# Kernel tuning notes

Measured on AMD Instinct MI355X. Metric: run time of the kernel, lower is better.

## Reference

```python
import jax, jax.numpy as jnp
import numpy as np

N, E, S, K, NB = 16384, 262144, 10, 64, 8
R_MAX, P_CUT, AVG_NEIGH = 5.0, 5, 16.0
L_OF_LM = np.array([0, 1, 1, 1, 2, 2, 2, 2, 2])  # l value of each of the 9 lm components
L_SLICES = [(0, 1), (1, 4), (4, 9)]               # lm ranges for l = 0,1,2
MLP_H = 16


def _sph(u):
    # real spherical harmonics up to l=2, e3nn 'component' normalization (sum_m Y_lm^2 = 2l+1)
    x, y, z = u[..., 0], u[..., 1], u[..., 2]
    s3, s15, s5 = np.float32(np.sqrt(3.0)), np.float32(np.sqrt(15.0)), np.float32(np.sqrt(5.0))
    return jnp.stack([
        jnp.ones_like(x),
        s3 * x, s3 * y, s3 * z,
        s15 * x * y, s15 * y * z, (s5 / 2) * (3 * z * z - 1), s15 * x * z, (s15 / 2) * (x * x - y * y),
    ], axis=-1)


def _radial(r):
    # Bessel radial basis with smooth polynomial cutoff envelope (p = P_CUT)
    u = r / R_MAX
    r_safe = jnp.where(r > 1e-9, r, 1.0)
    n = jnp.arange(1, NB + 1, dtype=r.dtype)
    bess = np.float32(np.sqrt(2.0 / R_MAX)) * jnp.sin(n * jnp.pi * u[:, None]) / r_safe[:, None]
    p = float(P_CUT)
    env = 1.0 - (p + 1) * (p + 2) / 2 * u**P_CUT + p * (p + 2) * u**(P_CUT + 1) - p * (p + 1) / 2 * u**(P_CUT + 2)
    env = jnp.where(u < 1.0, env, 0.0)
    return bess * env[:, None]  # [E, NB]


def setup_inputs() -> dict:
    key = jax.random.key(0)
    ks = jax.random.split(key, 16)
    positions = jax.random.uniform(ks[0], (N, 3), jnp.float32) * 4.0  # box so many edges fall inside r_max
    species = jax.random.randint(ks[1], (N,), 0, S)
    senders = jax.random.randint(ks[2], (E,), 0, N)
    receivers = jax.random.randint(ks[3], (E,), 0, N)
    shifts = jnp.zeros((E, 3), jnp.float32)
    W_embed = jax.random.normal(ks[4], (S, K), jnp.float32)
    W_rad = jax.random.normal(ks[5], (2, 3, NB, K), jnp.float32) * 0.3
    W_mix = jax.random.normal(ks[6], (2, 3, K, K), jnp.float32) / np.sqrt(K)
    W_prod = jax.random.normal(ks[7], (2, 3, 3, K), jnp.float32) * 0.1
    W_sc = jax.random.normal(ks[8], (2, S, 3, K, K), jnp.float32) / np.sqrt(K)
    W_ro0 = jax.random.normal(ks[9], (K,), jnp.float32) / np.sqrt(K)
    W_m1 = jax.random.normal(ks[10], (K, MLP_H), jnp.float32) / np.sqrt(K)
    b_m1 = jnp.zeros((MLP_H,), jnp.float32)
    W_m2 = jax.random.normal(ks[11], (MLP_H,), jnp.float32) / np.sqrt(MLP_H)
    return dict(positions=positions, shifts=shifts, species=species, senders=senders,
                receivers=receivers, W_embed=W_embed, W_rad=W_rad, W_mix=W_mix,
                W_prod=W_prod, W_sc=W_sc, W_ro0=W_ro0, W_m1=W_m1, b_m1=b_m1, W_m2=W_m2)


def reference(positions, shifts, species, senders, receivers, W_embed, W_rad, W_mix,
              W_prod, W_sc, W_ro0, W_m1, b_m1, W_m2):
    lm = jnp.asarray(L_OF_LM)
    onehot = jax.nn.one_hot(species, S, dtype=positions.dtype)
    # node embedding: scalars only -> feats [N, 9(lm), K]
    feats = jnp.zeros((N, 9, K), positions.dtype).at[:, 0, :].set(onehot @ W_embed)

    # edge geometry
    vec = positions[receivers] - positions[senders] + shifts           # [E, 3]
    r = jnp.linalg.norm(vec, axis=-1)                                  # [E]
    u_hat = vec / jnp.where(r > 1e-9, r, 1.0)[:, None]
    Y = _sph(u_hat)                                                     # [E, 9]
    rad = _radial(r)                                                    # [E, NB]

    energies = []
    for i in range(2):
        # interaction: radial-weighted SH messages from sender scalars, scatter-sum to receivers
        hs = feats[:, 0, :][senders]                                    # [E, K]
        Rl = jnp.einsum('eb,lbk->elk', rad, W_rad[i])[:, lm, :]         # [E, 9, K]
        msg = hs[:, None, :] * Y[:, :, None] * Rl                       # [E, 9, K]
        A = jax.ops.segment_sum(msg, receivers, num_segments=N) / AVG_NEIGH
        A = jnp.einsum('nmk,mkj->nmj', A, W_mix[i][lm])                 # per-l channel mixing

        # correlation-3 equivariant product basis (symmetric-contraction style)
        A0 = A[:, 0, :]
        inv = jnp.sum(A * A, axis=1)                                    # rotation-invariant [N, K]
        w1, w2, w3 = (W_prod[i, j][lm] for j in range(3))               # each [9, K]
        B = A * (w1[None] + w2[None] * A0[:, None, :] + w3[None] * inv[:, None, :])

        # species-dependent self-connection (linear of feats x node_attrs), per-l weights
        sc = jnp.concatenate([
            jnp.einsum('nmk,ns,skj->nmj', feats[:, st:en], onehot, W_sc[i, :, l])
            for l, (st, en) in enumerate(L_SLICES)], axis=1)
        feats = B + sc

        if i == 0:
            energies.append(feats[:, 0, :] @ W_ro0)                     # linear readout
        else:
            feats = feats.at[:, 1:, :].set(0.0)                         # last layer keeps 0e only
            energies.append(jax.nn.silu(feats[:, 0, :] @ W_m1 + b_m1) @ W_m2)

    return jnp.stack(energies, axis=1)  # [N, num_interactions]
```

## Files before the change

kernel.cpp:

```cpp
#include <hip/hip_runtime.h>

#define NN 16384
#define NE 262144
#define NSPEC 10
#define KC 64
#define MLPH 16
#define SEG 128
#define EPSG 2048
#define SC_BPS 160

typedef float v2f __attribute__((ext_vector_type(2)));

__device__ __forceinline__ float wave_reduce(float v) {
#pragma unroll
    for (int off = 32; off > 0; off >>= 1) v += __shfl_down(v, off, 64);
    return v;
}

__device__ __forceinline__ float f4c(const float4& v, int j) {
    const float* p = &v.x;
    return p[j];
}

__global__ void __launch_bounds__(1024) k_pre(
    const float* __restrict__ W_embed,
    const int* __restrict__ species,
    const int* __restrict__ receivers,
    int* __restrict__ eslot,
    unsigned short* __restrict__ cnt16,
    float4* __restrict__ h04) {
    __shared__ int cntL[NN];
    int t = threadIdx.x;
#pragma unroll
    for (int i = 0; i < 16; ++i) cntL[t + 1024 * i] = 0;
    __syncthreads();
    int ebase = blockIdx.x * EPSG;
#pragma unroll
    for (int j = 0; j < EPSG / 1024; ++j) {
        int e = ebase + j * 1024 + t;
        int r = receivers[e];
        eslot[e] = atomicAdd(&cntL[r], 1);
    }
    int gt = blockIdx.x * 1024 + t;
#pragma unroll
    for (int q = 0; q < 2; ++q) {
        int idx = gt * 2 + q;
        int n = idx >> 4, w = idx & 15;
        h04[idx] = reinterpret_cast<const float4*>(W_embed + species[n] * KC)[w];
    }
    __syncthreads();
    unsigned short* o = cnt16 + (size_t)blockIdx.x * NN;
#pragma unroll
    for (int i = 0; i < 16; ++i)
        o[t + 1024 * i] = (unsigned short)cntL[t + 1024 * i];
}

__global__ void __launch_bounds__(128) k_colscan(
    const unsigned short* __restrict__ cnt16,
    int* __restrict__ seg_base,
    int* __restrict__ count) {
    int r = blockIdx.x * 128 + threadIdx.x;
    int run = 0;
#pragma unroll 4
    for (int g = 0; g < SEG; ++g) {
        int c = cnt16[(size_t)g * NN + r];
        seg_base[(size_t)g * NN + r] = run;
        run += c;
    }
    count[r] = run;
}

__global__ void __launch_bounds__(1024) k_scan(
    const int* __restrict__ count, int* __restrict__ row_start,
    const int* __restrict__ species, int* __restrict__ nslot,
    int* __restrict__ sp_start) {
    __shared__ int lds[1024];
    __shared__ int itercnt[256 * NSPEC];
    __shared__ int spt[NSPEC];
    int t = threadIdx.x;
    int lane = t & 63;
    int w = t >> 6;
#pragma unroll
    for (int j = 0; j < 16; ++j) {
        int n = w * 1024 + j * 64 + lane;
        int sp = species[n];
#pragma unroll
        for (int s = 0; s < NSPEC; ++s) {
            unsigned long long mask = __ballot(sp == s);
            if (lane == 0) itercnt[(w * 16 + j) * NSPEC + s] = (int)__popcll(mask);
        }
    }
    int base = t * 16;
    int local[16];
    int ssum = 0;
#pragma unroll
    for (int b = 0; b < 16; ++b) { local[b] = count[base + b]; ssum += local[b]; }
    lds[t] = ssum;
    __syncthreads();
    for (int off = 1; off < 1024; off <<= 1) {
        int v = (t >= off) ? lds[t - off] : 0;
        __syncthreads();
        lds[t] += v;
        __syncthreads();
    }
    int run = lds[t] - ssum;
#pragma unroll
    for (int b = 0; b < 16; ++b) { row_start[base + b] = run; run += local[b]; }
    if (t == 1023) row_start[NN] = run;
    __syncthreads();
    if (w < NSPEC) {
        int s = w;
        int v0 = itercnt[(lane * 4 + 0) * NSPEC + s];
        int v1 = itercnt[(lane * 4 + 1) * NSPEC + s];
        int v2 = itercnt[(lane * 4 + 2) * NSPEC + s];
        int v3 = itercnt[(lane * 4 + 3) * NSPEC + s];
        int ls = v0 + v1 + v2 + v3;
        int inc = ls;
#pragma unroll
        for (int off = 1; off < 64; off <<= 1) {
            int v = __shfl_up(inc, off, 64);
            if (lane >= off) inc += v;
        }
        int exc = inc - ls;
        itercnt[(lane * 4 + 0) * NSPEC + s] = exc;
        itercnt[(lane * 4 + 1) * NSPEC + s] = exc + v0;
        itercnt[(lane * 4 + 2) * NSPEC + s] = exc + v0 + v1;
        itercnt[(lane * 4 + 3) * NSPEC + s] = exc + v0 + v1 + v2;
        if (lane == 63) spt[s] = inc;
    }
    __syncthreads();
    if (t == 0) {
        int r2 = 0;
        for (int s = 0; s < NSPEC; ++s) { sp_start[s] = r2; r2 += spt[s]; }
        sp_start[NSPEC] = r2;
    }
    __syncthreads();
#pragma unroll
    for (int j = 0; j < 16; ++j) {
        int n = w * 1024 + j * 64 + lane;
        int sp = species[n];
        int rank = 0;
#pragma unroll
        for (int s = 0; s < NSPEC; ++s) {
            unsigned long long mask = __ballot(sp == s);
            if (sp == s)
                rank = (int)__popcll(mask & ((1ull << lane) - 1ull));
        }
        nslot[n] = itercnt[(w * 16 + j) * NSPEC + sp] + rank;
    }
}

__global__ void k_geom(const float* __restrict__ pos,
                       const float* __restrict__ shifts,
                       const int* __restrict__ senders,
                       const int* __restrict__ receivers,
                       const int* __restrict__ row_start,
                       const int* __restrict__ seg_base,
                       const int* __restrict__ eslot,
                       const int* __restrict__ species,
                       const int* __restrict__ sp_start,
                       const int* __restrict__ nslot,
                       int* __restrict__ ord,
                       float* __restrict__ edgerec,
                       int* __restrict__ ssend) {
    int e = blockIdx.x * 256 + threadIdx.x;
    if (e < NN) {
        int sp = species[e];
        ord[sp_start[sp] + nslot[e]] = e;
    }
    int s = senders[e], r = receivers[e];
    float dx = pos[r * 3 + 0] - pos[s * 3 + 0] + shifts[e * 3 + 0];
    float dy = pos[r * 3 + 1] - pos[s * 3 + 1] + shifts[e * 3 + 1];
    float dz = pos[r * 3 + 2] - pos[s * 3 + 2] + shifts[e * 3 + 2];
    float rn = sqrtf(dx * dx + dy * dy + dz * dz);
    float den = (rn > 1e-9f) ? rn : 1.0f;
    float x = dx / den, y = dy / den, z = dz / den;
    const float s3  = 1.7320508075688772f;
    const float s15 = 3.8729833462074170f;
    const float s5h = 1.1180339887498949f;
    const float s15h = 1.9364916731037085f;
    float rec[16];
    rec[0] = s3 * x;
    rec[1] = s3 * y;
    rec[2] = s3 * z;
    rec[3] = s15 * x * y;
    rec[4] = s15 * y * z;
    rec[5] = s5h * (3.0f * z * z - 1.0f);
    rec[6] = s15 * x * z;
    rec[7] = s15h * (x * x - y * y);
    float u = rn * 0.2f;
    float env = 0.0f;
    if (u < 1.0f) {
        float u2 = u * u;
        float u5 = u2 * u2 * u;
        env = 1.0f - 21.0f * u5 + 35.0f * u5 * u - 15.0f * u5 * u2;
    }
    float pre = 0.63245553203367587f * env / den;
    float half_u = 0.5f * u;
#pragma unroll
    for (int nb = 1; nb <= 8; ++nb) {
        float tr = (float)nb * half_u;
        tr -= floorf(tr);
        rec[7 + nb] = pre * __builtin_amdgcn_sinf(tr);
    }
    int p = row_start[r] + seg_base[(size_t)(e >> 11) * NN + r] + eslot[e];
    float4* o = (float4*)(edgerec + (size_t)p * 16);
#pragma unroll
    for (int i = 0; i < 4; ++i)
        o[i] = make_float4(rec[4 * i], rec[4 * i + 1], rec[4 * i + 2], rec[4 * i + 3]);
    ssend[p] = s;
}

__device__ __forceinline__ void agg_edge_pk(
    const float* __restrict__ rc, float hv,
    const float (&Wr0)[8], const v2f (&Wr12)[8],
    float& acc0, v2f (&accp)[4]) {
    float R0 = 0.f;
    v2f R12 = (v2f){0.f, 0.f};
#pragma unroll
    for (int b = 0; b < 8; ++b) {
        float rb = rc[8 + b];
        R0 = fmaf(rb, Wr0[b], R0);
        R12 = __builtin_elementwise_fma((v2f){rb, rb}, Wr12[b], R12);
    }
    acc0 = fmaf(hv, R0, acc0);
    float t1 = hv * R12.x, t2 = hv * R12.y;
    accp[0] = __builtin_elementwise_fma((v2f){t1, t1}, (v2f){rc[0], rc[1]}, accp[0]);
    accp[1] = __builtin_elementwise_fma((v2f){t1, t2}, (v2f){rc[2], rc[3]}, accp[1]);
    accp[2] = __builtin_elementwise_fma((v2f){t2, t2}, (v2f){rc[4], rc[5]}, accp[2]);
    accp[3] = __builtin_elementwise_fma((v2f){t2, t2}, (v2f){rc[6], rc[7]}, accp[3]);
}

__global__ void __launch_bounds__(512, 6) k_aggmix(
    const float* __restrict__ h,
    const float* __restrict__ edgerec,
    const int* __restrict__ ssend,
    const int* __restrict__ row_start,
    const float* __restrict__ Wr_i,
    const float* __restrict__ Wm_i,
    const float* __restrict__ Wp_i,
    float* __restrict__ Bm0) {
    __shared__ float Wlds[2 * 4096];
    __shared__ float xtile[8][9 * 64];
    {
        float4* Wl4 = (float4*)Wlds;
        const float4* W4 = (const float4*)(Wm_i + 4096);
#pragma unroll
        for (int i = 0; i < 4; ++i)
            Wl4[threadIdx.x + 512 * i] = W4[threadIdx.x + 512 * i];
    }
    __syncthreads();
    int lane = threadIdx.x & 63;
    int wid = __builtin_amdgcn_readfirstlane(threadIdx.x >> 6);
    float* xt = xtile[wid];
    float Wr0[8];
    v2f  Wr12[8];
#pragma unroll
    for (int b = 0; b < 8; ++b) {
        Wr0[b]    = Wr_i[b * 64 + lane] * (1.0f / 16.0f);
        Wr12[b].x = Wr_i[(8 + b) * 64 + lane] * (1.0f / 16.0f);
        Wr12[b].y = Wr_i[(16 + b) * 64 + lane] * (1.0f / 16.0f);
    }
    float w10 = Wp_i[0 * 64 + lane];
    float w20 = Wp_i[3 * 64 + lane];
    float w30 = Wp_i[6 * 64 + lane];
    const float* W0g = Wm_i;

    int nA = (blockIdx.x * 8 + wid) * 2;
    int nB = nA + 1;
    int eA0 = row_start[nA], eA1 = row_start[nA + 1], eB1 = row_start[nB + 1];
    int eB0 = eA1;
    int cA = eA1 - eA0, cB = eB1 - eB0;
    int mc = min(cA, cB);

    float accA0 = 0.f, accB0 = 0.f;
    v2f accAp[4], accBp[4];
#pragma unroll
    for (int q = 0; q < 4; ++q) { accAp[q] = (v2f){0.f, 0.f}; accBp[q] = (v2f){0.f, 0.f}; }

#pragma unroll 2
    for (int i = 0; i < mc; ++i) {
        int ea = eA0 + i, eb = eB0 + i;
        int sa = ssend[ea], sb = ssend[eb];
        float ha = h[(size_t)sa * 64 + lane];
        float hb = h[(size_t)sb * 64 + lane];
        const float* ra = edgerec + (size_t)ea * 16;
        const float* rb = edgerec + (size_t)eb * 16;
        agg_edge_pk(ra, ha, Wr0, Wr12, accA0, accAp);
        agg_edge_pk(rb, hb, Wr0, Wr12, accB0, accBp);
    }
#pragma unroll 2
    for (int i = mc; i < cA; ++i) {
        int ea = eA0 + i;
        int sa = ssend[ea];
        float ha = h[(size_t)sa * 64 + lane];
        agg_edge_pk(edgerec + (size_t)ea * 16, ha, Wr0, Wr12, accA0, accAp);
    }
#pragma unroll 2
    for (int i = mc; i < cB; ++i) {
        int eb = eB0 + i;
        int sb = ssend[eb];
        float hb = h[(size_t)sb * 64 + lane];
        agg_edge_pk(edgerec + (size_t)eb * 16, hb, Wr0, Wr12, accB0, accBp);
    }

#pragma unroll
    for (int nn = 0; nn < 2; ++nn) {
        float a0 = nn ? accB0 : accA0;
        v2f* ap = nn ? accBp : accAp;
        int n = nn ? nB : nA;
        xt[0 * 64 + lane] = a0;
        xt[1 * 64 + lane] = ap[0].x;  xt[2 * 64 + lane] = ap[0].y;
        xt[3 * 64 + lane] = ap[1].x;  xt[4 * 64 + lane] = ap[1].y;
        xt[5 * 64 + lane] = ap[2].x;  xt[6 * 64 + lane] = ap[2].y;
        xt[7 * 64 + lane] = ap[3].x;  xt[8 * 64 + lane] = ap[3].y;
        v2f mixp[9];
#pragma unroll
        for (int m = 0; m < 9; ++m) mixp[m] = (v2f){0.f, 0.f};
#pragma unroll 2
        for (int c4 = 0; c4 < 16; ++c4) {
            float4 xb[9];
#pragma unroll
            for (int m = 0; m < 9; ++m)
                xb[m] = *(const float4*)&xt[m * 64 + c4 * 4];
#pragma unroll
            for (int j2 = 0; j2 < 2; ++j2) {
                int k0 = c4 * 4 + j2 * 2;
                v2f wv0 = (v2f){W0g[k0 * 64 + lane], W0g[(k0 + 1) * 64 + lane]};
                v2f wv1 = (v2f){Wlds[k0 * 64 + lane], Wlds[(k0 + 1) * 64 + lane]};
                v2f wv2 = (v2f){Wlds[4096 + k0 * 64 + lane], Wlds[4096 + (k0 + 1) * 64 + lane]};
#pragma unroll
                for (int m = 0; m < 9; ++m) {
                    v2f xp = (v2f){f4c(xb[m], j2 * 2), f4c(xb[m], j2 * 2 + 1)};
                    v2f wv = (m == 0) ? wv0 : ((m < 4) ? wv1 : wv2);
                    mixp[m] = __builtin_elementwise_fma(xp, wv, mixp[m]);
                }
            }
        }
        float mix[9];
#pragma unroll
        for (int m = 0; m < 9; ++m) mix[m] = mixp[m].x + mixp[m].y;
        float A0 = mix[0];
        float inv = 0.f;
#pragma unroll
        for (int m = 0; m < 9; ++m) inv += mix[m] * mix[m];
        Bm0[(size_t)n * 64 + lane] = mix[0] * (w10 + w20 * A0 + w30 * inv);
    }
}

#define RPB 32
template <int ITER>
__global__ void __launch_bounds__(256) k_sc(
    const float* __restrict__ h_in,
    const float* __restrict__ Bm0,
    float* __restrict__ h_out,
    const int* __restrict__ ord,
    const int* __restrict__ sp_start,
    const float* __restrict__ Wsc_i,
    const float* __restrict__ W_ro0,
    const float* __restrict__ W_m1,
    const float* __restrict__ b_m1,
    const float* __restrict__ W_m2,
    float* __restrict__ out) {
    int sp = blockIdx.x / SC_BPS;
    int c  = blockIdx.x - sp * SC_BPS;
    int base = sp_start[sp];
    int cnt  = sp_start[sp + 1] - base;
    int r0 = c * RPB;
    __shared__ float Wlds[4096];
    __shared__ float xtile[4][8 * 64];
    if (r0 < cnt) {
        const float4* W4 = (const float4*)(Wsc_i + (size_t)sp * 3 * 4096);
        float4* Wl4 = (float4*)Wlds;
#pragma unroll
        for (int i = 0; i < 4; ++i)
            Wl4[threadIdx.x + 256 * i] = W4[threadIdx.x + 256 * i];
    }
    __syncthreads();
    if (r0 >= cnt) return;
    int lane = threadIdx.x & 63;
    int wid = threadIdx.x >> 6;
    float* xt = xtile[wid];
    int rend = min(r0 + RPB, cnt);
    int q0 = r0 + wid * 8;
    if (q0 >= rend) return;
    int nd[8];
#pragma unroll
    for (int t = 0; t < 8; ++t)
        nd[t] = ord[base + min(q0 + t, rend - 1)];
    float xv[8];
#pragma unroll
    for (int t = 0; t < 8; ++t) xv[t] = h_in[(size_t)nd[t] * 64 + lane];
#pragma unroll
    for (int t = 0; t < 8; ++t) xt[t * 64 + lane] = xv[t];
    float acc[8];
#pragma unroll
    for (int t = 0; t < 8; ++t) acc[t] = 0.f;
#pragma unroll 2
    for (int c4 = 0; c4 < 16; ++c4) {
        float wv[4];
#pragma unroll
        for (int j = 0; j < 4; ++j) wv[j] = Wlds[(c4 * 4 + j) * 64 + lane];
#pragma unroll
        for (int t = 0; t < 8; ++t) {
            float4 xb = *(const float4*)&xt[t * 64 + c4 * 4];
#pragma unroll
            for (int j = 0; j < 4; ++j) acc[t] += f4c(xb, j) * wv[j];
        }
    }
    float wro = W_ro0[lane];
#pragma unroll
    for (int t = 0; t < 8; ++t) {
        if (q0 + t >= rend) break;
        int node = nd[t];
        float outv = acc[t] + Bm0[(size_t)node * 64 + lane];
        if (ITER == 0) {
            h_out[(size_t)node * 64 + lane] = outv;
            float e = wave_reduce(outv * wro);
            if (lane == 0) out[2 * node + 0] = e;
        } else {
            int hh = lane & 15;
            float tacc = b_m1[hh];
#pragma unroll
            for (int k = 0; k < 64; ++k)
                tacc += __shfl(outv, k, 64) * W_m1[k * MLPH + hh];
            float sig = 1.0f / (1.0f + expf(-tacc));
            float contrib = (lane < MLPH) ? tacc * sig * W_m2[lane] : 0.f;
            float e = wave_reduce(contrib);
            if (lane == 0) out[2 * node + 1] = e;
        }
    }
}

extern "C" void kernel_launch(void* const* d_in, const int* in_sizes, int n_in,
                              void* d_out, int out_size, void* d_ws, size_t ws_size,
                              hipStream_t stream) {
    const float* positions = (const float*)d_in[0];
    const float* shifts    = (const float*)d_in[1];
    const int*   species   = (const int*)d_in[2];
    const int*   senders   = (const int*)d_in[3];
    const int*   receivers = (const int*)d_in[4];
    const float* W_embed   = (const float*)d_in[5];
    const float* W_rad     = (const float*)d_in[6];
    const float* W_mix     = (const float*)d_in[7];
    const float* W_prod    = (const float*)d_in[8];
    const float* W_sc      = (const float*)d_in[9];
    const float* W_ro0     = (const float*)d_in[10];
    const float* W_m1      = (const float*)d_in[11];
    const float* b_m1      = (const float*)d_in[12];
    const float* W_m2      = (const float*)d_in[13];
    float* out = (float*)d_out;

    char* p = (char*)d_ws;
    float* edgerec = (float*)p; p += (size_t)NE * 16 * 4;
    int* seg_base  = (int*)p;   p += (size_t)SEG * NN * 4;
    float* Bm0     = (float*)p; p += (size_t)NN * KC * 4;
    float* h0      = (float*)p; p += (size_t)NN * KC * 4;
    float* h1      = (float*)p; p += (size_t)NN * KC * 4;
    unsigned short* cnt16 = (unsigned short*)p; p += (size_t)SEG * NN * 2;
    int* eslot     = (int*)p; p += (size_t)NE * 4;
    int* ssend     = (int*)p; p += (size_t)NE * 4;
    int* nslot     = (int*)p; p += (size_t)NN * 4;
    int* ord       = (int*)p; p += (size_t)NN * 4;
    int* count     = (int*)p; p += (size_t)NN * 4;
    int* row_start = (int*)p; p += (size_t)(NN + 1) * 4;
    int* sp_start  = (int*)p; p += 16 * 4;

    k_pre<<<SEG, 1024, 0, stream>>>(W_embed, species, receivers,
                                    eslot, cnt16, (float4*)h0);
    k_colscan<<<NN / 128, 128, 0, stream>>>(cnt16, seg_base, count);
    k_scan<<<1, 1024, 0, stream>>>(count, row_start, species, nslot, sp_start);
    k_geom<<<NE / 256, 256, 0, stream>>>(positions, shifts, senders, receivers,
                                         row_start, seg_base, eslot, species,
                                         sp_start, nslot, ord, edgerec, ssend);

    k_aggmix<<<NN / 16, 512, 0, stream>>>(h0, edgerec, ssend, row_start,
        W_rad + 0, W_mix + 0, W_prod + 0, Bm0);
    k_sc<0><<<NSPEC * SC_BPS, 256, 0, stream>>>(h0, Bm0, h1, ord, sp_start,
        W_sc + 0, W_ro0, W_m1, b_m1, W_m2, out);

    k_aggmix<<<NN / 16, 512, 0, stream>>>(h1, edgerec, ssend, row_start,
        W_rad + 1536, W_mix + 12288, W_prod + 576, Bm0);
    k_sc<1><<<NSPEC * SC_BPS, 256, 0, stream>>>(h1, Bm0, h0 , ord,
        sp_start, W_sc + (size_t)NSPEC * 3 * 4096, W_ro0, W_m1, b_m1, W_m2, out);
}
```

Before: 273.4 us.

## Fuse species self-connection and readout into aggregation kernel, drop species sort

The separate k_sc kernel, which grouped nodes by species and did the self-connection matmul from an LDS-staged weight tile, is folded into k_aggmix. Each wave now computes its node's self-connection directly from global W_sc rows indexed by that node's species, then runs the readout. The species bucketing (ord/nslot/sp_start) in k_scan and k_geom and the Bm0 intermediate buffer are removed. This saves two launches, the Bm0 round trip and the sort work, at the cost of uncoalesced per-node reads of a 16KB weight slice through cache instead of LDS reuse.

```diff
diff --git a/kernel.cpp b/kernel.cpp
--- a/kernel.cpp
+++ b/kernel.cpp
@@ -7,7 +7,6 @@
 #define MLPH 16
 #define SEG 128
 #define EPSG 2048
-#define SC_BPS 160
 
 typedef float v2f __attribute__((ext_vector_type(2)));
 
@@ -71,25 +70,9 @@
 }
 
 __global__ void __launch_bounds__(1024) k_scan(
-    const int* __restrict__ count, int* __restrict__ row_start,
-    const int* __restrict__ species, int* __restrict__ nslot,
-    int* __restrict__ sp_start) {
+    const int* __restrict__ count, int* __restrict__ row_start) {
     __shared__ int lds[1024];
-    __shared__ int itercnt[256 * NSPEC];
-    __shared__ int spt[NSPEC];
     int t = threadIdx.x;
-    int lane = t & 63;
-    int w = t >> 6;
-#pragma unroll
-    for (int j = 0; j < 16; ++j) {
-        int n = w * 1024 + j * 64 + lane;
-        int sp = species[n];
-#pragma unroll
-        for (int s = 0; s < NSPEC; ++s) {
-            unsigned long long mask = __ballot(sp == s);
-            if (lane == 0) itercnt[(w * 16 + j) * NSPEC + s] = (int)__popcll(mask);
-        }
-    }
     int base = t * 16;
     int local[16];
     int ssum = 0;
@@ -107,47 +90,6 @@
 #pragma unroll
     for (int b = 0; b < 16; ++b) { row_start[base + b] = run; run += local[b]; }
     if (t == 1023) row_start[NN] = run;
-    __syncthreads();
-    if (w < NSPEC) {
-        int s = w;
-        int v0 = itercnt[(lane * 4 + 0) * NSPEC + s];
-        int v1 = itercnt[(lane * 4 + 1) * NSPEC + s];
-        int v2 = itercnt[(lane * 4 + 2) * NSPEC + s];
-        int v3 = itercnt[(lane * 4 + 3) * NSPEC + s];
-        int ls = v0 + v1 + v2 + v3;
-        int inc = ls;
-#pragma unroll
-        for (int off = 1; off < 64; off <<= 1) {
-            int v = __shfl_up(inc, off, 64);
-            if (lane >= off) inc += v;
-        }
-        int exc = inc - ls;
-        itercnt[(lane * 4 + 0) * NSPEC + s] = exc;
-        itercnt[(lane * 4 + 1) * NSPEC + s] = exc + v0;
-        itercnt[(lane * 4 + 2) * NSPEC + s] = exc + v0 + v1;
-        itercnt[(lane * 4 + 3) * NSPEC + s] = exc + v0 + v1 + v2;
-        if (lane == 63) spt[s] = inc;
-    }
-    __syncthreads();
-    if (t == 0) {
-        int r2 = 0;
-        for (int s = 0; s < NSPEC; ++s) { sp_start[s] = r2; r2 += spt[s]; }
-        sp_start[NSPEC] = r2;
-    }
-    __syncthreads();
-#pragma unroll
-    for (int j = 0; j < 16; ++j) {
-        int n = w * 1024 + j * 64 + lane;
-        int sp = species[n];
-        int rank = 0;
-#pragma unroll
-        for (int s = 0; s < NSPEC; ++s) {
-            unsigned long long mask = __ballot(sp == s);
-            if (sp == s)
-                rank = (int)__popcll(mask & ((1ull << lane) - 1ull));
-        }
-        nslot[n] = itercnt[(w * 16 + j) * NSPEC + sp] + rank;
-    }
 }
 
 __global__ void k_geom(const float* __restrict__ pos,
@@ -157,17 +99,9 @@
                        const int* __restrict__ row_start,
                        const int* __restrict__ seg_base,
                        const int* __restrict__ eslot,
-                       const int* __restrict__ species,
-                       const int* __restrict__ sp_start,
-                       const int* __restrict__ nslot,
-                       int* __restrict__ ord,
                        float* __restrict__ edgerec,
                        int* __restrict__ ssend) {
     int e = blockIdx.x * 256 + threadIdx.x;
-    if (e < NN) {
-        int sp = species[e];
-        ord[sp_start[sp] + nslot[e]] = e;
-    }
     int s = senders[e], r = receivers[e];
     float dx = pos[r * 3 + 0] - pos[s * 3 + 0] + shifts[e * 3 + 0];
     float dy = pos[r * 3 + 1] - pos[s * 3 + 1] + shifts[e * 3 + 1];
@@ -231,15 +165,23 @@
     accp[3] = __builtin_elementwise_fma((v2f){t2, t2}, (v2f){rc[6], rc[7]}, accp[3]);
 }
 
+template <int ITER>
 __global__ void __launch_bounds__(512, 6) k_aggmix(
     const float* __restrict__ h,
     const float* __restrict__ edgerec,
     const int* __restrict__ ssend,
     const int* __restrict__ row_start,
+    const int* __restrict__ species,
     const float* __restrict__ Wr_i,
     const float* __restrict__ Wm_i,
     const float* __restrict__ Wp_i,
-    float* __restrict__ Bm0) {
+    const float* __restrict__ Wsc_i,
+    const float* __restrict__ W_ro0,
+    const float* __restrict__ W_m1,
+    const float* __restrict__ b_m1,
+    const float* __restrict__ W_m2,
+    float* __restrict__ h_out,
+    float* __restrict__ out) {
     __shared__ float Wlds[2 * 4096];
     __shared__ float xtile[8][9 * 64];
     {
@@ -264,6 +206,7 @@
     float w10 = Wp_i[0 * 64 + lane];
     float w20 = Wp_i[3 * 64 + lane];
     float w30 = Wp_i[6 * 64 + lane];
+    float wro = (ITER == 0) ? W_ro0[lane] : 0.f;
     const float* W0g = Wm_i;
 
     int nA = (blockIdx.x * 8 + wid) * 2;
@@ -337,87 +280,37 @@
                 }
             }
         }
-        float mix[9];
-#pragma unroll
-        for (int m = 0; m < 9; ++m) mix[m] = mixp[m].x + mixp[m].y;
-        float A0 = mix[0];
-        float inv = 0.f;
-#pragma unroll
-        for (int m = 0; m < 9; ++m) inv += mix[m] * mix[m];
-        Bm0[(size_t)n * 64 + lane] = mix[0] * (w10 + w20 * A0 + w30 * inv);
-    }
-}
-
-#define RPB 32
-template <int ITER>
-__global__ void __launch_bounds__(256) k_sc(
-    const float* __restrict__ h_in,
-    const float* __restrict__ Bm0,
-    float* __restrict__ h_out,
-    const int* __restrict__ ord,
-    const int* __restrict__ sp_start,
-    const float* __restrict__ Wsc_i,
-    const float* __restrict__ W_ro0,
-    const float* __restrict__ W_m1,
-    const float* __restrict__ b_m1,
-    const float* __restrict__ W_m2,
-    float* __restrict__ out) {
-    int sp = blockIdx.x / SC_BPS;
-    int c  = blockIdx.x - sp * SC_BPS;
-    int base = sp_start[sp];
-    int cnt  = sp_start[sp + 1] - base;
-    int r0 = c * RPB;
-    __shared__ float Wlds[4096];
-    __shared__ float xtile[4][8 * 64];
-    if (r0 < cnt) {
-        const float4* W4 = (const float4*)(Wsc_i + (size_t)sp * 3 * 4096);
-        float4* Wl4 = (float4*)Wlds;
-#pragma unroll
-        for (int i = 0; i < 4; ++i)
-            Wl4[threadIdx.x + 256 * i] = W4[threadIdx.x + 256 * i];
-    }
-    __syncthreads();
-    if (r0 >= cnt) return;
-    int lane = threadIdx.x & 63;
-    int wid = threadIdx.x >> 6;
-    float* xt = xtile[wid];
-    int rend = min(r0 + RPB, cnt);
-    int q0 = r0 + wid * 8;
-    if (q0 >= rend) return;
-    int nd[8];
-#pragma unroll
-    for (int t = 0; t < 8; ++t)
-        nd[t] = ord[base + min(q0 + t, rend - 1)];
-    float xv[8];
-#pragma unroll
-    for (int t = 0; t < 8; ++t) xv[t] = h_in[(size_t)nd[t] * 64 + lane];
-#pragma unroll
-    for (int t = 0; t < 8; ++t) xt[t * 64 + lane] = xv[t];
-    float acc[8];
-#pragma unroll
-    for (int t = 0; t < 8; ++t) acc[t] = 0.f;
-#pragma unroll 2
-    for (int c4 = 0; c4 < 16; ++c4) {
-        float wv[4];
-#pragma unroll
-        for (int j = 0; j < 4; ++j) wv[j] = Wlds[(c4 * 4 + j) * 64 + lane];
-#pragma unroll
-        for (int t = 0; t < 8; ++t) {
-            float4 xb = *(const float4*)&xt[t * 64 + c4 * 4];
-#pragma unroll
-            for (int j = 0; j < 4; ++j) acc[t] += f4c(xb, j) * wv[j];
+        float mix0 = mixp[0].x + mixp[0].y;
+        float A0 = mix0;
+        v2f invp = (v2f){0.f, 0.f};
+#pragma unroll
+        for (int m = 0; m < 9; ++m)
+            invp = __builtin_elementwise_fma(mixp[m], mixp[m], invp);
+        float inv = invp.x + invp.y;
+        float B0 = mix0 * (w10 + w20 * A0 + w30 * inv);
+
+        int spn = species[n];
+        const float* Wsp = Wsc_i + (size_t)spn * 3 * 4096;
+        float hown = h[(size_t)n * 64 + lane];
+        xt[lane] = hown;
+        v2f accs = (v2f){0.f, 0.f};
+#pragma unroll 4
+        for (int c4 = 0; c4 < 16; ++c4) {
+            float4 xb = *(const float4*)&xt[c4 * 4];
+            int k0 = c4 * 4;
+            accs = __builtin_elementwise_fma(
+                (v2f){xb.x, xb.y},
+                (v2f){Wsp[k0 * 64 + lane], Wsp[(k0 + 1) * 64 + lane]}, accs);
+            accs = __builtin_elementwise_fma(
+                (v2f){xb.z, xb.w},
+                (v2f){Wsp[(k0 + 2) * 64 + lane], Wsp[(k0 + 3) * 64 + lane]}, accs);
         }
-    }
-    float wro = W_ro0[lane];
-#pragma unroll
-    for (int t = 0; t < 8; ++t) {
-        if (q0 + t >= rend) break;
-        int node = nd[t];
-        float outv = acc[t] + Bm0[(size_t)node * 64 + lane];
+        float outv = accs.x + accs.y + B0;
+
         if (ITER == 0) {
-            h_out[(size_t)node * 64 + lane] = outv;
+            h_out[(size_t)n * 64 + lane] = outv;
             float e = wave_reduce(outv * wro);
-            if (lane == 0) out[2 * node + 0] = e;
+            if (lane == 0) out[2 * n + 0] = e;
         } else {
             int hh = lane & 15;
             float tacc = b_m1[hh];
@@ -427,7 +320,7 @@
             float sig = 1.0f / (1.0f + expf(-tacc));
             float contrib = (lane < MLPH) ? tacc * sig * W_m2[lane] : 0.f;
             float e = wave_reduce(contrib);
-            if (lane == 0) out[2 * node + 1] = e;
+            if (lane == 0) out[2 * n + 1] = e;
         }
     }
 }
@@ -454,33 +347,28 @@
     char* p = (char*)d_ws;
     float* edgerec = (float*)p; p += (size_t)NE * 16 * 4;
     int* seg_base  = (int*)p;   p += (size_t)SEG * NN * 4;
-    float* Bm0     = (float*)p; p += (size_t)NN * KC * 4;
     float* h0      = (float*)p; p += (size_t)NN * KC * 4;
     float* h1      = (float*)p; p += (size_t)NN * KC * 4;
     unsigned short* cnt16 = (unsigned short*)p; p += (size_t)SEG * NN * 2;
     int* eslot     = (int*)p; p += (size_t)NE * 4;
     int* ssend     = (int*)p; p += (size_t)NE * 4;
-    int* nslot     = (int*)p; p += (size_t)NN * 4;
-    int* ord       = (int*)p; p += (size_t)NN * 4;
     int* count     = (int*)p; p += (size_t)NN * 4;
     int* row_start = (int*)p; p += (size_t)(NN + 1) * 4;
-    int* sp_start  = (int*)p; p += 16 * 4;
 
     k_pre<<<SEG, 1024, 0, stream>>>(W_embed, species, receivers,
                                     eslot, cnt16, (float4*)h0);
     k_colscan<<<NN / 128, 128, 0, stream>>>(cnt16, seg_base, count);
-    k_scan<<<1, 1024, 0, stream>>>(count, row_start, species, nslot, sp_start);
+    k_scan<<<1, 1024, 0, stream>>>(count, row_start);
     k_geom<<<NE / 256, 256, 0, stream>>>(positions, shifts, senders, receivers,
-                                         row_start, seg_base, eslot, species,
-                                         sp_start, nslot, ord, edgerec, ssend);
-
-    k_aggmix<<<NN / 16, 512, 0, stream>>>(h0, edgerec, ssend, row_start,
-        W_rad + 0, W_mix + 0, W_prod + 0, Bm0);
-    k_sc<0><<<NSPEC * SC_BPS, 256, 0, stream>>>(h0, Bm0, h1, ord, sp_start,
-        W_sc + 0, W_ro0, W_m1, b_m1, W_m2, out);
-
-    k_aggmix<<<NN / 16, 512, 0, stream>>>(h1, edgerec, ssend, row_start,
-        W_rad + 1536, W_mix + 12288, W_prod + 576, Bm0);
-    k_sc<1><<<NSPEC * SC_BPS, 256, 0, stream>>>(h1, Bm0, h0 , ord,
-        sp_start, W_sc + (size_t)NSPEC * 3 * 4096, W_ro0, W_m1, b_m1, W_m2, out);
-}
+                                         row_start, seg_base, eslot,
+                                         edgerec, ssend);
+
+    k_aggmix<0><<<NN / 16, 512, 0, stream>>>(h0, edgerec, ssend, row_start,
+        species, W_rad + 0, W_mix + 0, W_prod + 0, W_sc + 0,
+        W_ro0, W_m1, b_m1, W_m2, h1, out);
+
+    k_aggmix<1><<<NN / 16, 512, 0, stream>>>(h1, edgerec, ssend, row_start,
+        species, W_rad + 1536, W_mix + 12288, W_prod + 576,
+        W_sc + (size_t)NSPEC * 3 * 4096,
+        W_ro0, W_m1, b_m1, W_m2, h0 , out);
+}
```

New measurement: 356.0 us. 30.2% more time.
